# Kernel tuning notes

Measured on AMD Instinct MI355X. Metric: run time of the kernel, lower is better.

## Reference

```python
import jax, jax.numpy as jnp
import numpy as np

BATCH = 2048
FID_NUM = 65536
AVG_ACTIVE = 20.0  # ~active fids per example


def setup_inputs() -> dict:
    key = jax.random.key(0)
    k1, k2, k3 = jax.random.split(key, 3)
    # binary one-hot gate, ~AVG_ACTIVE ones per row (matches _get_model_feed_dict)
    gate = (jax.random.uniform(k1, (BATCH, FID_NUM)) < (AVG_ACTIVE / FID_NUM)).astype(jnp.float32)
    sparse_bias = 0.01 * jax.random.normal(k2, (FID_NUM,), dtype=jnp.float32)
    global_bias = jnp.zeros((1,), dtype=jnp.float32)
    label = (jax.random.uniform(k3, (BATCH,)) < 0.5).astype(jnp.float32)
    return {"bias_fid_gate": gate, "sparse_bias": sparse_bias,
            "global_bias": global_bias, "label": label}


def reference(bias_fid_gate, sparse_bias, global_bias, label):
    # bias_input = gate * bias; logits = reduce_sum(bias_input, axis=1) + global_bias
    logits = jnp.sum(bias_fid_gate * sparse_bias, axis=1) + global_bias[0]  # [B]
    pred = jax.nn.sigmoid(logits)
    # tf.nn.sigmoid_cross_entropy_with_logits, then reduce_sum
    per_ex = jnp.maximum(logits, 0.0) - logits * label + jnp.log1p(jnp.exp(-jnp.abs(logits)))
    loss = jnp.sum(per_ex)
    return logits, pred, loss
```

## Files before the change

### kernel.cpp

```cpp
#include <hip/hip_runtime.h>
#include <math.h>

#define BATCH 2048
#define FID 65536
#define NT 256
#define ROWS 4
#define NV (FID / 4)

typedef float vf4 __attribute__((ext_vector_type(4)));

__global__ __launch_bounds__(NT) void lr_rows(
        const float* __restrict__ gate,
        const float* __restrict__ bias,
        const float* __restrict__ gbias,
        float* __restrict__ out) {
    const int r0 = blockIdx.x * ROWS;
    const vf4* __restrict__ b4 = (const vf4*)bias;
    const vf4* __restrict__ g4 = (const vf4*)gate + (size_t)r0 * NV;

    float a0 = 0.f, a1 = 0.f, a2 = 0.f, a3 = 0.f;

    #pragma unroll 2
    for (int i = threadIdx.x; i < NV; i += NT) {
        vf4 v  = b4[i];
        vf4 g0 = __builtin_nontemporal_load(&g4[i]);
        vf4 g1 = __builtin_nontemporal_load(&g4[i + NV]);
        vf4 g2 = __builtin_nontemporal_load(&g4[i + 2 * NV]);
        vf4 g3 = __builtin_nontemporal_load(&g4[i + 3 * NV]);
        a0 = fmaf(g0.x, v.x, a0); a0 = fmaf(g0.y, v.y, a0);
        a0 = fmaf(g0.z, v.z, a0); a0 = fmaf(g0.w, v.w, a0);
        a1 = fmaf(g1.x, v.x, a1); a1 = fmaf(g1.y, v.y, a1);
        a1 = fmaf(g1.z, v.z, a1); a1 = fmaf(g1.w, v.w, a1);
        a2 = fmaf(g2.x, v.x, a2); a2 = fmaf(g2.y, v.y, a2);
        a2 = fmaf(g2.z, v.z, a2); a2 = fmaf(g2.w, v.w, a2);
        a3 = fmaf(g3.x, v.x, a3); a3 = fmaf(g3.y, v.y, a3);
        a3 = fmaf(g3.w, v.w, a3); a3 = fmaf(g3.z, v.z, a3);
    }

    #pragma unroll
    for (int off = 32; off > 0; off >>= 1) {
        a0 += __shfl_down(a0, off, 64);
        a1 += __shfl_down(a1, off, 64);
        a2 += __shfl_down(a2, off, 64);
        a3 += __shfl_down(a3, off, 64);
    }

    __shared__ float wsum[NT / 64][ROWS];
    const int wave = threadIdx.x >> 6;
    const int lane = threadIdx.x & 63;
    if (lane == 0) {
        wsum[wave][0] = a0; wsum[wave][1] = a1;
        wsum[wave][2] = a2; wsum[wave][3] = a3;
    }
    __syncthreads();

    if (threadIdx.x < ROWS) {
        const int r = threadIdx.x;
        float s = wsum[0][r] + wsum[1][r] + wsum[2][r] + wsum[3][r];
        float logit = s + gbias[0];
        out[r0 + r] = logit;
        out[BATCH + r0 + r] = 1.0f / (1.0f + expf(-logit));
    }
}

__global__ __launch_bounds__(NT) void lr_loss(
        const float* __restrict__ out_logits,
        const float* __restrict__ label,
        float* __restrict__ loss_out) {
    float acc = 0.0f;
    for (int i = threadIdx.x; i < BATCH; i += NT) {
        float x = out_logits[i];
        float l = label[i];
        acc += fmaxf(x, 0.0f) - x * l + log1pf(expf(-fabsf(x)));
    }
    #pragma unroll
    for (int off = 32; off > 0; off >>= 1)
        acc += __shfl_down(acc, off, 64);

    __shared__ float wsum[NT / 64];
    const int wave = threadIdx.x >> 6;
    const int lane = threadIdx.x & 63;
    if (lane == 0) wsum[wave] = acc;
    __syncthreads();
    if (threadIdx.x == 0)
        loss_out[0] = wsum[0] + wsum[1] + wsum[2] + wsum[3];
}

extern "C" void kernel_launch(void* const* d_in, const int* in_sizes, int n_in,
                              void* d_out, int out_size, void* d_ws, size_t ws_size,
                              hipStream_t stream) {
    const float* gate  = (const float*)d_in[0];
    const float* bias  = (const float*)d_in[1];
    const float* gbias = (const float*)d_in[2];
    const float* label = (const float*)d_in[3];
    float* out = (float*)d_out;

    lr_rows<<<BATCH / ROWS, NT, 0, stream>>>(gate, bias, gbias, out);
    lr_loss<<<1, NT, 0, stream>>>(out, label, out + 2 * BATCH);
}
```

Baseline: 666.2 us.

## Split row reduction across K with atomic partial sums and deeper unroll

Each group of four rows is now processed by two blocks, each covering half the feature dimension, which doubles the grid size. Partial sums are combined with atomicAdd into a zeroed output, and the bias, sigmoid and loss are moved into the final single-block kernel. The loop unroll is raised to keep more loads in flight. This adds a memset launch and atomics, and the accumulation order changes slightly.

```diff
diff --git a/kernel.cpp b/kernel.cpp
--- a/kernel.cpp
+++ b/kernel.cpp
@@ -6,22 +6,27 @@
 #define NT 256
 #define ROWS 4
 #define NV (FID / 4)
+#define KSPLIT 2
+#define NVH (NV / KSPLIT)
 
 typedef float vf4 __attribute__((ext_vector_type(4)));
 
-__global__ __launch_bounds__(NT) void lr_rows(
+__global__ __launch_bounds__(NT) void lr_partial(
         const float* __restrict__ gate,
         const float* __restrict__ bias,
-        const float* __restrict__ gbias,
         float* __restrict__ out) {
-    const int r0 = blockIdx.x * ROWS;
+    const int kb = blockIdx.x & (KSPLIT - 1);
+    const int rb = blockIdx.x >> 1;
+    const int r0 = rb * ROWS;
     const vf4* __restrict__ b4 = (const vf4*)bias;
     const vf4* __restrict__ g4 = (const vf4*)gate + (size_t)r0 * NV;
+    const int i0 = kb * NVH;
+    const int i1 = i0 + NVH;
 
     float a0 = 0.f, a1 = 0.f, a2 = 0.f, a3 = 0.f;
 
-    #pragma unroll 2
-    for (int i = threadIdx.x; i < NV; i += NT) {
+    #pragma unroll 4
+    for (int i = i0 + threadIdx.x; i < i1; i += NT) {
         vf4 v  = b4[i];
         vf4 g0 = __builtin_nontemporal_load(&g4[i]);
         vf4 g1 = __builtin_nontemporal_load(&g4[i + NV]);
@@ -34,7 +39,7 @@
         a2 = fmaf(g2.x, v.x, a2); a2 = fmaf(g2.y, v.y, a2);
         a2 = fmaf(g2.z, v.z, a2); a2 = fmaf(g2.w, v.w, a2);
         a3 = fmaf(g3.x, v.x, a3); a3 = fmaf(g3.y, v.y, a3);
-        a3 = fmaf(g3.w, v.w, a3); a3 = fmaf(g3.z, v.z, a3);
+        a3 = fmaf(g3.z, v.z, a3); a3 = fmaf(g3.w, v.w, a3);
     }
 
     #pragma unroll
@@ -57,20 +62,21 @@
     if (threadIdx.x < ROWS) {
         const int r = threadIdx.x;
         float s = wsum[0][r] + wsum[1][r] + wsum[2][r] + wsum[3][r];
-        float logit = s + gbias[0];
-        out[r0 + r] = logit;
-        out[BATCH + r0 + r] = 1.0f / (1.0f + expf(-logit));
+        atomicAdd(&out[r0 + r], s);
     }
 }
 
-__global__ __launch_bounds__(NT) void lr_loss(
-        const float* __restrict__ out_logits,
+__global__ __launch_bounds__(NT) void lr_finish(
+        const float* __restrict__ gbias,
         const float* __restrict__ label,
-        float* __restrict__ loss_out) {
+        float* __restrict__ out) {
+    const float gb = gbias[0];
     float acc = 0.0f;
     for (int i = threadIdx.x; i < BATCH; i += NT) {
-        float x = out_logits[i];
+        float x = out[i] + gb;
         float l = label[i];
+        out[i] = x;
+        out[BATCH + i] = 1.0f / (1.0f + expf(-x));
         acc += fmaxf(x, 0.0f) - x * l + log1pf(expf(-fabsf(x)));
     }
     #pragma unroll
@@ -83,7 +89,7 @@
     if (lane == 0) wsum[wave] = acc;
     __syncthreads();
     if (threadIdx.x == 0)
-        loss_out[0] = wsum[0] + wsum[1] + wsum[2] + wsum[3];
+        out[2 * BATCH] = wsum[0] + wsum[1] + wsum[2] + wsum[3];
 }
 
 extern "C" void kernel_launch(void* const* d_in, const int* in_sizes, int n_in,
@@ -95,6 +101,8 @@
     const float* label = (const float*)d_in[3];
     float* out = (float*)d_out;
 
-    lr_rows<<<BATCH / ROWS, NT, 0, stream>>>(gate, bias, gbias, out);
-    lr_loss<<<1, NT, 0, stream>>>(out, label, out + 2 * BATCH);
+    hipMemsetAsync(out, 0, BATCH * sizeof(float), stream);
+
+    lr_partial<<<(BATCH / ROWS) * KSPLIT, NT, 0, stream>>>(gate, bias, out);
+    lr_finish<<<1, NT, 0, stream>>>(gbias, label, out);
 }
```

New measurement: 650.3 us. 1.02x faster.
